# Optimization experiments

Hardware: AMD Instinct MI355X
Metric: run time of the kernel (lower is better)

The kernel has to match this reference:

```python
import jax, jax.numpy as jnp
import numpy as np

WH, WW = 7, 7
N = WH * WW
DIM = 384
HEADS = 12
NW = 64          # windows per image
B_ = 2048        # batch * NW


def _relative_position_index():
    ch, cw = np.meshgrid(np.arange(WH), np.arange(WW), indexing='ij')
    coords = np.stack([ch, cw]).reshape(2, -1)                      # [2, N]
    rel = coords[:, :, None] - coords[:, None, :]                   # [2, N, N]
    rel = rel.transpose(1, 2, 0)
    rel[:, :, 0] += WH - 1
    rel[:, :, 1] += WW - 1
    rel[:, :, 0] *= 2 * WW - 1
    return jnp.asarray(rel.sum(-1), dtype=jnp.int32)                # [N, N]


def setup_inputs() -> dict:
    key = jax.random.key(0)
    ks = jax.random.split(key, 7)
    return {
        'x': jax.random.normal(ks[0], (B_, N, DIM), dtype=jnp.float32),
        'qkv_w': jax.random.normal(ks[1], (3 * DIM, DIM), dtype=jnp.float32) * 0.02,
        'qkv_b': jax.random.normal(ks[2], (3 * DIM,), dtype=jnp.float32) * 0.02,
        'proj_w': jax.random.normal(ks[3], (DIM, DIM), dtype=jnp.float32) * 0.02,
        'proj_b': jax.random.normal(ks[4], (DIM,), dtype=jnp.float32) * 0.02,
        'bias_table': jax.random.normal(ks[5], ((2 * WH - 1) * (2 * WW - 1), HEADS), dtype=jnp.float32) * 0.02,
        'mask': jax.random.normal(ks[6], (NW, N, N), dtype=jnp.float32),
        'rel_idx': _relative_position_index(),
    }


def reference(x, qkv_w, qkv_b, proj_w, proj_b, bias_table, mask, rel_idx):
    B_, n, C = x.shape
    H = HEADS
    hd = C // H
    scale = hd ** (-0.5)

    qkv = x @ qkv_w.T + qkv_b                                        # [B_, N, 3C]
    qkv = qkv.reshape(B_, n, 3, H, hd).transpose(2, 0, 3, 1, 4)      # [3, B_, H, N, hd]
    q, k, v = qkv[0], qkv[1], qkv[2]

    attn = jnp.einsum('bhqd,bhkd->bhqk', q * scale, k)               # [B_, H, N, N]

    rpb = bias_table[rel_idx.reshape(-1)].reshape(n, n, H)           # gather [N, N, H]
    attn = attn + rpb.transpose(2, 0, 1)[None]                       # [B_, H, N, N]

    nW = mask.shape[0]
    attn = attn.reshape(B_ // nW, nW, H, n, n) + mask[None, :, None]
    attn = attn.reshape(B_, H, n, n)
    attn = jax.nn.softmax(attn, axis=-1)

    out = jnp.einsum('bhqk,bhkd->bhqd', attn, v)                     # [B_, H, N, hd]
    out = out.transpose(0, 2, 1, 3).reshape(B_, n, C)
    return out @ proj_w.T + proj_b
```

## Files before the change

kernel.cpp:

```cpp
#include <hip/hip_runtime.h>
#include <hip/hip_bf16.h>
#include <cstdint>
#include <cstddef>

#define NTOK 49
#define DIM 384
#define KDIM 384
#define HEADS 12
#define HD 32
#define BATCH 2048
#define MROWS (BATCH * NTOK)

typedef unsigned short u16;
typedef __bf16 bf16x8 __attribute__((ext_vector_type(8)));
typedef unsigned short u16x8 __attribute__((ext_vector_type(8)));
typedef float f32x4 __attribute__((ext_vector_type(4)));

__device__ __forceinline__ u16 f2b(float f) {
  union { float f; unsigned u; } v; v.f = f;
  unsigned r = v.u + 0x7fffu + ((v.u >> 16) & 1u);
  return (u16)(r >> 16);
}

__device__ __forceinline__ bf16x8 ld_bf8(const u16* p) {
  u16x8 u = *(const u16x8*)p;
  return __builtin_bit_cast(bf16x8, u);
}

__device__ __forceinline__ void gload_lds16(const void* g, void* l) {
  __builtin_amdgcn_global_load_lds(
      (const __attribute__((address_space(1))) unsigned*)g,
      (__attribute__((address_space(3))) unsigned*)l, 16, 0, 0);
}

__global__ __launch_bounds__(256) void k_prep(const float* __restrict__ x,
                                              u16* __restrict__ xb,
                                              const float* __restrict__ qkv_w,
                                              u16* __restrict__ wqkvb,
                                              const float* __restrict__ proj_w,
                                              u16* __restrict__ wprojb,
                                              const float* __restrict__ bias_table,
                                              const float* __restrict__ mask,
                                              const int* __restrict__ rel_idx,
                                              float* __restrict__ rpbm) {
  int blk = blockIdx.x;
  if (blk < 38208) {
    const float* in;
    u16* out;
    int i;
    if (blk < 37632) {
      in = x; out = xb; i = blk * 256 + threadIdx.x;
    } else if (blk < 38064) {
      in = qkv_w; out = wqkvb; i = (blk - 37632) * 256 + threadIdx.x;
    } else {
      in = proj_w; out = wprojb; i = (blk - 38064) * 256 + threadIdx.x;
    }
    float4 v = ((const float4*)in)[i];
    ushort4 o;
    o.x = f2b(v.x); o.y = f2b(v.y); o.z = f2b(v.z); o.w = f2b(v.w);
    ((ushort4*)out)[i] = o;
  } else {
    int idx = (blk - 38208) * 256 + threadIdx.x;
    int r  = idx & 3;
    int l  = (idx >> 2) & 63;
    int ni = (idx >> 8) & 3;
    int mi = (idx >> 10) & 3;
    int w  = (idx >> 12) & 63;
    int h  = idx >> 18;
    int row = mi * 16 + (l >> 4) * 4 + r;
    int col = ni * 16 + (l & 15);
    float v = -1e30f;
    if (row < NTOK && col < NTOK)
      v = bias_table[rel_idx[row * NTOK + col] * HEADS + h] +
          mask[(w * NTOK + row) * NTOK + col];
    rpbm[idx] = v;
  }
}

template <int OUT_BF16, int NCOLS, int NTN, int GD8>
__global__ __launch_bounds__(256) void k_gemm(const u16* __restrict__ A,
                                              const u16* __restrict__ B,
                                              const float* __restrict__ bias,
                                              void* __restrict__ Cv) {
  __shared__ u16 sh[16384];
  int bid = blockIdx.x;
  int tile = (bid & 7) * GD8 + (bid >> 3);
  int mt = tile / NTN, nt = tile - mt * NTN;
  long m0 = (long)mt * 128;
  int n0 = nt * 128;
  int tid = threadIdx.x;
  int lane = tid & 63, wid = tid >> 6;
  int wr = (wid >> 1) * 64, wc = (wid & 1) * 64;
  int c = lane & 15, g = lane >> 4;

  int srow = wid * 16 + (lane >> 2);
  int scol = (lane & 3) * 8;
  const u16* gA = A + (m0 + srow) * (long)KDIM + scol;
  const u16* gB = B + (long)(n0 + srow) * KDIM + scol;

  f32x4 acc[4][4] = {};

  auto STAGE = [&](int buf, int ktS) {
    u16* As = sh + buf * 8192;
    u16* Bs = As + 4096;
    gload_lds16(gA + ktS, &As[srow * 32 + scol]);
    gload_lds16(gA + ktS + 64L * KDIM, &As[(srow + 64) * 32 + scol]);
    gload_lds16(gB + ktS, &Bs[srow * 32 + scol]);
    gload_lds16(gB + ktS + 64L * KDIM, &Bs[(srow + 64) * 32 + scol]);
  };

  STAGE(0, 0);
  __syncthreads();
  int cur = 0;
  for (int kt = 0; kt < KDIM; kt += 32) {
    if (kt + 32 < KDIM) STAGE(cur ^ 1, kt + 32);
    const u16* As = sh + cur * 8192;
    const u16* Bs = As + 4096;
    bf16x8 af[4], bfr[4];
#pragma unroll
    for (int i = 0; i < 4; ++i) {
      af[i]  = ld_bf8(&As[(wr + i * 16 + c) * 32 + g * 8]);
      bfr[i] = ld_bf8(&Bs[(wc + i * 16 + c) * 32 + g * 8]);
    }
#pragma unroll
    for (int mi = 0; mi < 4; ++mi)
#pragma unroll
      for (int ni = 0; ni < 4; ++ni)
        acc[mi][ni] = __builtin_amdgcn_mfma_f32_16x16x32_bf16(
            af[mi], bfr[ni], acc[mi][ni], 0, 0, 0);
    __syncthreads();
    cur ^= 1;
  }

  if (OUT_BF16) {
    u16* C = (u16*)Cv;
#pragma unroll
    for (int mi = 0; mi < 4; ++mi)
#pragma unroll
      for (int ni = 0; ni < 4; ++ni) {
        int col = wc + ni * 16 + c;
        float bv = bias[n0 + col];
#pragma unroll
        for (int r = 0; r < 4; ++r) {
          int row = wr + mi * 16 + g * 4 + r;
          sh[row * 128 + col] = f2b(acc[mi][ni][r] + bv);
        }
      }
    __syncthreads();
#pragma unroll
    for (int rep = 0; rep < 8; ++rep) {
      int idx = rep * 2048 + tid * 8;
      int row = idx >> 7, col = idx & 127;
      *(u16x8*)(C + (m0 + row) * NCOLS + n0 + col) = *(const u16x8*)&sh[idx];
    }
  } else {
    float* C = (float*)Cv;
    float* shf = (float*)sh;
#pragma unroll
    for (int chunk = 0; chunk < 2; ++chunk) {
      __syncthreads();
      if ((wr >> 6) == chunk) {
#pragma unroll
        for (int mi = 0; mi < 4; ++mi)
#pragma unroll
          for (int ni = 0; ni < 4; ++ni) {
            int col = wc + ni * 16 + c;
            float bv = bias[n0 + col];
#pragma unroll
            for (int r = 0; r < 4; ++r) {
              int lrow = mi * 16 + g * 4 + r;
              shf[lrow * 128 + col] = acc[mi][ni][r] + bv;
            }
          }
      }
      __syncthreads();
#pragma unroll
      for (int rep = 0; rep < 8; ++rep) {
        int idx = rep * 1024 + tid * 4;
        int row = idx >> 7, col = idx & 127;
        *(float4*)(C + (m0 + chunk * 64 + row) * NCOLS + n0 + col) =
            *(const float4*)&shf[idx];
      }
    }
  }
}

__global__ __launch_bounds__(256) void k_attn(const u16* __restrict__ qkv,
                                              const float* __restrict__ rpbm,
                                              u16* __restrict__ attnout) {
  __shared__ u16 P_lds[4][64 * 64];
  __shared__ u16 vT_lds[4][32 * 64];
  int lane = threadIdx.x & 63, wid = threadIdx.x >> 6;
  int blk = blockIdx.x;
  int w = blk / 96;
  int rr = blk - w * 96;
  int j = rr / 3;
  int hb = rr - j * 3;
  int b = j * 64 + w;
  int h = hb * 4 + wid;
  const u16* base = qkv + (size_t)b * (NTOK * 1152);
  int c = lane & 15, g = lane >> 4;

  u16* vt = vT_lds[wid];
  {
    const u16* vbase = base + 2 * DIM + h * HD;
#pragma unroll
    for (int t = 0; t < 4; ++t) {
      int idx = t * 64 + lane;
      int jj = idx >> 2, d0 = (idx & 3) * 8;
      int jr = jj < NTOK ? jj : NTOK - 1;
      u16x8 vv = *(const u16x8*)(vbase + (size_t)jr * 1152 + d0);
#pragma unroll
      for (int dd = 0; dd < 8; ++dd) {
        int d = d0 + dd;
        int byte = (d * 128 + jj * 2) ^ ((d & 7) << 4);
        *(u16*)((char*)vt + byte) = (u16)vv[dd];
      }
    }
  }

  bf16x8 qa[4], kb[4];
#pragma unroll
  for (int mi = 0; mi < 4; ++mi) {
    int row = mi * 16 + c; if (row > NTOK - 1) row = NTOK - 1;
    qa[mi] = ld_bf8(base + (size_t)row * 1152 + h * HD + g * 8);
  }
#pragma unroll
  for (int ni = 0; ni < 4; ++ni) {
    int row = ni * 16 + c; if (row > NTOK - 1) row = NTOK - 1;
    kb[ni] = ld_bf8(base + (size_t)row * 1152 + DIM + h * HD + g * 8);
  }

  f32x4 s[4][4] = {};
#pragma unroll
  for (int mi = 0; mi < 4; ++mi)
#pragma unroll
    for (int ni = 0; ni < 4; ++ni)
      s[mi][ni] = __builtin_amdgcn_mfma_f32_16x16x32_bf16(qa[mi], kb[ni],
                                                          s[mi][ni], 0, 0, 0);

  const float scale = 0.17677669529663687f;
  const f32x4* rp = (const f32x4*)(rpbm + ((size_t)(h * 64 + w)) * 4096);
#pragma unroll
  for (int mi = 0; mi < 4; ++mi)
#pragma unroll
    for (int ni = 0; ni < 4; ++ni) {
      f32x4 rv = rp[(mi * 4 + ni) * 64 + lane];
#pragma unroll
      for (int r = 0; r < 4; ++r)
        s[mi][ni][r] = s[mi][ni][r] * scale + rv[r];
    }

#pragma unroll
  for (int mi = 0; mi < 4; ++mi)
#pragma unroll
    for (int r = 0; r < 4; ++r) {
      float mx = fmaxf(fmaxf(s[mi][0][r], s[mi][1][r]),
                       fmaxf(s[mi][2][r], s[mi][3][r]));
      mx = fmaxf(mx, __shfl_xor(mx, 1));
      mx = fmaxf(mx, __shfl_xor(mx, 2));
      mx = fmaxf(mx, __shfl_xor(mx, 4));
      mx = fmaxf(mx, __shfl_xor(mx, 8));
      float sum = 0.f;
#pragma unroll
      for (int ni = 0; ni < 4; ++ni) {
        float p = __expf(s[mi][ni][r] - mx);
        s[mi][ni][r] = p;
        sum += p;
      }
      sum += __shfl_xor(sum, 1);
      sum += __shfl_xor(sum, 2);
      sum += __shfl_xor(sum, 4);
      sum += __shfl_xor(sum, 8);
      float inv = __builtin_amdgcn_rcpf(sum);
#pragma unroll
      for (int ni = 0; ni < 4; ++ni) s[mi][ni][r] *= inv;
    }

  u16* pl = P_lds[wid];
#pragma unroll
  for (int mi = 0; mi < 4; ++mi)
#pragma unroll
    for (int ni = 0; ni < 4; ++ni) {
      int col = ni * 16 + c;
#pragma unroll
      for (int r = 0; r < 4; ++r) {
        int row = mi * 16 + g * 4 + r;
        int byte = (row * 128 + col * 2) ^ ((row & 7) << 4);
        *(u16*)((char*)pl + byte) = f2b(s[mi][ni][r]);
      }
    }
  asm volatile("s_waitcnt lgkmcnt(0)" ::: "memory");

  f32x4 o[4][2] = {};
#pragma unroll
  for (int ks = 0; ks < 2; ++ks) {
    bf16x8 vb[2];
#pragma unroll
    for (int n2 = 0; n2 < 2; ++n2) {
      int d = n2 * 16 + c;
      int byte = (d * 128 + ks * 64 + g * 16) ^ ((d & 7) << 4);
      vb[n2] = __builtin_bit_cast(bf16x8, *(const u16x8*)((const char*)vt + byte));
    }
#pragma unroll
    for (int mi = 0; mi < 4; ++mi) {
      int row = mi * 16 + c;
      int byte = (row * 128 + ks * 64 + g * 16) ^ ((row & 7) << 4);
      bf16x8 pa = __builtin_bit_cast(bf16x8, *(const u16x8*)((const char*)pl + byte));
#pragma unroll
      for (int n2 = 0; n2 < 2; ++n2)
        o[mi][n2] = __builtin_amdgcn_mfma_f32_16x16x32_bf16(pa, vb[n2],
                                                            o[mi][n2], 0, 0, 0);
    }
  }

  u16* obase = attnout + (size_t)b * (NTOK * DIM) + h * HD;
#pragma unroll
  for (int mi = 0; mi < 4; ++mi)
#pragma unroll
    for (int r = 0; r < 4; ++r) {
      int row = mi * 16 + g * 4 + r;
      if (row < NTOK) {
#pragma unroll
        for (int n2 = 0; n2 < 2; ++n2)
          obase[(size_t)row * DIM + n2 * 16 + c] = f2b(o[mi][n2][r]);
      }
    }
}

extern "C" void kernel_launch(void* const* d_in, const int* in_sizes, int n_in,
                              void* d_out, int out_size, void* d_ws, size_t ws_size,
                              hipStream_t stream) {
  const float* x       = (const float*)d_in[0];
  const float* qkv_w   = (const float*)d_in[1];
  const float* qkv_b   = (const float*)d_in[2];
  const float* proj_w  = (const float*)d_in[3];
  const float* proj_b  = (const float*)d_in[4];
  const float* bias_tb = (const float*)d_in[5];
  const float* mask    = (const float*)d_in[6];
  const int*   rel_idx = (const int*)d_in[7];
  float* out = (float*)d_out;

  char* ws = (char*)d_ws;
  u16*   xb      = (u16*)(ws + 0);
  u16*   wqkvb   = (u16*)(ws + 77070336);
  u16*   wprojb  = (u16*)(ws + 77955072);
  float* rpbm    = (float*)(ws + 78249984);
  u16*   qkv     = (u16*)(ws + 90832896);
  u16*   attnout = (u16*)(ws + 322043904);

  k_prep<<<50496, 256, 0, stream>>>(x, xb, qkv_w, wqkvb, proj_w, wprojb,
                                    bias_tb, mask, rel_idx, rpbm);

  k_gemm<1, 1152, 9, 882><<<7056, 256, 0, stream>>>(xb, wqkvb, qkv_b, (void*)qkv);

  k_attn<<<6144, 256, 0, stream>>>(qkv, rpbm, attnout);

  k_gemm<0, 384, 3, 294><<<2352, 256, 0, stream>>>(attnout, wprojb, proj_b,
                                                   (void*)out);

  (void)in_sizes; (void)n_in; (void)out_size; (void)ws_size;
}
```

Baseline: 373.1 us.

## Triple-buffer GEMM K-loop with explicit vmcnt waits and full unroll

Replaces the double-buffered GEMM main loop with a three-stage LDS ring, prefetching two K-tiles ahead and fully unrolling the 12 iterations. Explicit s_waitcnt vmcnt counts let global-to-LDS loads stay in flight across iterations, and each buffer is refilled right after its fragments are read into registers. This aims to hide global load latency behind MFMA work, at the cost of more LDS per block, which may reduce occupancy, and two barriers per iteration.

```diff
diff --git a/kernel.cpp b/kernel.cpp
--- a/kernel.cpp
+++ b/kernel.cpp
@@ -82,7 +82,7 @@
                                               const u16* __restrict__ B,
                                               const float* __restrict__ bias,
                                               void* __restrict__ Cv) {
-  __shared__ u16 sh[16384];
+  __shared__ u16 sh[24576];
   int bid = blockIdx.x;
   int tile = (bid & 7) * GD8 + (bid >> 3);
   int mt = tile / NTN, nt = tile - mt * NTN;
@@ -100,37 +100,44 @@
 
   f32x4 acc[4][4] = {};
 
-  auto STAGE = [&](int buf, int ktS) {
-    u16* As = sh + buf * 8192;
-    u16* Bs = As + 4096;
-    gload_lds16(gA + ktS, &As[srow * 32 + scol]);
-    gload_lds16(gA + ktS + 64L * KDIM, &As[(srow + 64) * 32 + scol]);
-    gload_lds16(gB + ktS, &Bs[srow * 32 + scol]);
-    gload_lds16(gB + ktS + 64L * KDIM, &Bs[(srow + 64) * 32 + scol]);
-  };
+#define STAGE(BUF, KT)                                                         \
+  {                                                                            \
+    u16* As_ = sh + (BUF) * 8192;                                              \
+    u16* Bs_ = As_ + 4096;                                                     \
+    gload_lds16(gA + (KT), &As_[srow * 32 + scol]);                            \
+    gload_lds16(gA + (KT) + 64L * KDIM, &As_[(srow + 64) * 32 + scol]);        \
+    gload_lds16(gB + (KT), &Bs_[srow * 32 + scol]);                            \
+    gload_lds16(gB + (KT) + 64L * KDIM, &Bs_[(srow + 64) * 32 + scol]);        \
+  }
+
+#define GITER(T, NV)                                                           \
+  {                                                                            \
+    asm volatile("s_waitcnt vmcnt(" #NV ")" ::: "memory");                     \
+    __builtin_amdgcn_s_barrier();                                              \
+    const u16* As = sh + ((T) % 3) * 8192;                                     \
+    const u16* Bs = As + 4096;                                                 \
+    bf16x8 af[4], bfr[4];                                                      \
+    _Pragma("unroll") for (int i = 0; i < 4; ++i) {                            \
+      af[i]  = ld_bf8(&As[(wr + i * 16 + c) * 32 + g * 8]);                    \
+      bfr[i] = ld_bf8(&Bs[(wc + i * 16 + c) * 32 + g * 8]);                    \
+    }                                                                          \
+    asm volatile("s_waitcnt lgkmcnt(0)" ::: "memory");                         \
+    __builtin_amdgcn_s_barrier();                                              \
+    if ((T) + 3 < 12) STAGE((T) % 3, ((T) + 3) * 32);                          \
+    _Pragma("unroll") for (int mi = 0; mi < 4; ++mi)                           \
+    _Pragma("unroll") for (int ni = 0; ni < 4; ++ni)                           \
+        acc[mi][ni] = __builtin_amdgcn_mfma_f32_16x16x32_bf16(                 \
+            af[mi], bfr[ni], acc[mi][ni], 0, 0, 0);                            \
+  }
 
   STAGE(0, 0);
-  __syncthreads();
-  int cur = 0;
-  for (int kt = 0; kt < KDIM; kt += 32) {
-    if (kt + 32 < KDIM) STAGE(cur ^ 1, kt + 32);
-    const u16* As = sh + cur * 8192;
-    const u16* Bs = As + 4096;
-    bf16x8 af[4], bfr[4];
-#pragma unroll
-    for (int i = 0; i < 4; ++i) {
-      af[i]  = ld_bf8(&As[(wr + i * 16 + c) * 32 + g * 8]);
-      bfr[i] = ld_bf8(&Bs[(wc + i * 16 + c) * 32 + g * 8]);
-    }
-#pragma unroll
-    for (int mi = 0; mi < 4; ++mi)
-#pragma unroll
-      for (int ni = 0; ni < 4; ++ni)
-        acc[mi][ni] = __builtin_amdgcn_mfma_f32_16x16x32_bf16(
-            af[mi], bfr[ni], acc[mi][ni], 0, 0, 0);
-    __syncthreads();
-    cur ^= 1;
-  }
+  STAGE(1, 32);
+  STAGE(2, 64);
+  GITER(0, 8)  GITER(1, 8)  GITER(2, 8)  GITER(3, 8)
+  GITER(4, 8)  GITER(5, 8)  GITER(6, 8)  GITER(7, 8)
+  GITER(8, 8)  GITER(9, 8)  GITER(10, 4) GITER(11, 0)
+#undef GITER
+#undef STAGE
 
   if (OUT_BF16) {
     u16* C = (u16*)Cv;
```

After: 371.9 us. Within noise of the previous version (-0.3%).
